# Optimization experiments

Measured on AMD Instinct MI355X. Metric: run time of the kernel, lower is better.

The kernel has to match this reference:

```python
import jax, jax.numpy as jnp
import numpy as np

B, T, D, H, L, V = 16, 1024, 512, 8, 6, 96
HS = D // H
FF = 4 * D


def setup_inputs() -> dict:
    key = jax.random.key(0)
    ks = jax.random.split(key, 16)
    n = lambda k, shape: jax.random.normal(k, shape, jnp.float32) * 0.02
    return {
        "idx": jax.random.randint(ks[0], (B, T), 0, V),
        "targets": jax.random.randint(ks[1], (B, T), 0, V),
        "tok_emb": n(ks[2], (V, D)),
        "pos_emb": n(ks[3], (T, D)),
        "Wq": n(ks[4], (L, H, D, HS)),
        "Wk": n(ks[5], (L, H, D, HS)),
        "Wv": n(ks[6], (L, H, D, HS)),
        "Wproj": n(ks[7], (L, D, D)),
        "bproj": jnp.zeros((L, D), jnp.float32),
        "W1": n(ks[8], (L, D, FF)),
        "b1": jnp.zeros((L, FF), jnp.float32),
        "W2": n(ks[9], (L, FF, D)),
        "b2": jnp.zeros((L, D), jnp.float32),
        "ln1_s": jnp.ones((L, D), jnp.float32),
        "ln1_b": jnp.zeros((L, D), jnp.float32),
        "ln2_s": jnp.ones((L, D), jnp.float32),
        "ln2_b": jnp.zeros((L, D), jnp.float32),
        "lnf_s": jnp.ones((D,), jnp.float32),
        "lnf_b": jnp.zeros((D,), jnp.float32),
        "Wout": n(ks[10], (D, V)),
        "bout": jnp.zeros((V,), jnp.float32),
    }


def _ln(x, s, b, eps=1e-5):
    m = x.mean(-1, keepdims=True)
    v = ((x - m) ** 2).mean(-1, keepdims=True)
    return (x - m) * jax.lax.rsqrt(v + eps) * s + b


def reference(idx, targets, tok_emb, pos_emb, Wq, Wk, Wv, Wproj, bproj,
              W1, b1, W2, b2, ln1_s, ln1_b, ln2_s, ln2_b, lnf_s, lnf_b,
              Wout, bout):
    x = tok_emb[idx] + pos_emb[:T]  # [B,T,D]
    causal = jnp.tril(jnp.ones((T, T), jnp.bool_))
    scale = D ** (-0.5)  # NOTE: source scales by full channel dim, not head_size
    for l in range(L):
        h = _ln(x, ln1_s[l], ln1_b[l])
        q = jnp.einsum("btd,hdk->bhtk", h, Wq[l])
        k = jnp.einsum("btd,hdk->bhtk", h, Wk[l])
        v = jnp.einsum("btd,hdk->bhtk", h, Wv[l])
        att = jnp.einsum("bhtk,bhsk->bhts", q, k) * scale
        att = jnp.where(causal, att, -jnp.inf)
        att = jax.nn.softmax(att, axis=-1)
        o = jnp.einsum("bhts,bhsk->bhtk", att, v)
        o = o.transpose(0, 2, 1, 3).reshape(B, T, D)  # concat heads
        x = x + (o @ Wproj[l] + bproj[l])
        h2 = _ln(x, ln2_s[l], ln2_b[l])
        x = x + (jnp.maximum(h2 @ W1[l] + b1[l], 0.0) @ W2[l] + b2[l])
    x = _ln(x, lnf_s, lnf_b)
    logits = (x @ Wout + bout).reshape(B * T, V)
    logp = jax.nn.log_softmax(logits, axis=-1)
    loss = -logp[jnp.arange(B * T), targets.reshape(-1)].mean()
    return logits, loss
```

## Files before the change

### kernel.cpp

```cpp
#include <hip/hip_runtime.h>

#define B_  16
#define T_  1024
#define D_  512
#define H_  8
#define L_  6
#define V_  96
#define HS_ 64
#define FF_ 2048
#define BT_ (B_*T_)
#define QKS 1024

typedef __attribute__((ext_vector_type(8))) short bf16x8;
typedef __attribute__((ext_vector_type(4))) float f32x4;

typedef __attribute__((address_space(3))) unsigned int lds_u32_t;
typedef const __attribute__((address_space(1))) unsigned int glb_u32_t;

__device__ __forceinline__ void gload16(const unsigned short* g, unsigned short* l) {
  __builtin_amdgcn_global_load_lds((glb_u32_t*)g, (lds_u32_t*)l, 16, 0, 0);
}

__device__ __forceinline__ unsigned short f2b(float f) {
  unsigned u = __float_as_uint(f);
  unsigned r = (u + 0x7FFFu + ((u >> 16) & 1u)) >> 16;
  return (unsigned short)r;
}

__global__ void zero_kernel(float* p) { p[0] = 0.f; }

__global__ __launch_bounds__(128) void embed_kernel(const int* __restrict__ idx,
    const float* __restrict__ tok, const float* __restrict__ pos, float* __restrict__ x) {
  int bt = blockIdx.x;
  int t  = bt & (T_ - 1);
  int id = idx[bt];
  if (id < 0) id = 0; if (id > V_ - 1) id = V_ - 1;
  int d  = threadIdx.x * 4;
  float4 tv = *(const float4*)(tok + (size_t)id * D_ + d);
  float4 pv = *(const float4*)(pos + (size_t)t  * D_ + d);
  float4 o = {tv.x + pv.x, tv.y + pv.y, tv.z + pv.z, tv.w + pv.w};
  *(float4*)(x + (size_t)bt * D_ + d) = o;
}

__global__ __launch_bounds__(256) void transpose_cvt(const float* __restrict__ src,
    unsigned short* __restrict__ dst, int R, int C, long sstride, long dstride,
    int zper, long zouter) {
  __shared__ float t[32][33];
  const float* s = src + (size_t)blockIdx.z * sstride;
  unsigned short* d = dst + (size_t)(blockIdx.z / zper) * zouter
                          + (size_t)(blockIdx.z % zper) * dstride;
  int r0 = blockIdx.y * 32, c0 = blockIdx.x * 32;
  int tr = threadIdx.x >> 5, tc = threadIdx.x & 31;
#pragma unroll
  for (int i = 0; i < 4; ++i)
    t[tr + i * 8][tc] = s[(size_t)(r0 + tr + i * 8) * C + c0 + tc];
  __syncthreads();
#pragma unroll
  for (int i = 0; i < 4; ++i)
    d[(size_t)(c0 + tr + i * 8) * R + r0 + tc] = f2b(t[tc][tr + i * 8]);
}

template<bool BF16OUT>
__global__ __launch_bounds__(256) void ln_kernel(const float* __restrict__ x,
    const float* __restrict__ s, const float* __restrict__ b, void* __restrict__ outv) {
  int wave = threadIdx.x >> 6;
  int lane = threadIdx.x & 63;
  int r = blockIdx.x * 4 + wave;
  const float* xr = x + (size_t)r * D_;
  float vals[8];
  float sum = 0.f;
#pragma unroll
  for (int j = 0; j < 8; ++j) { vals[j] = xr[j * 64 + lane]; sum += vals[j]; }
#pragma unroll
  for (int o = 32; o > 0; o >>= 1) sum += __shfl_xor(sum, o, 64);
  float mean = sum * (1.f / D_);
  float vs = 0.f;
#pragma unroll
  for (int j = 0; j < 8; ++j) { float d = vals[j] - mean; vs += d * d; }
#pragma unroll
  for (int o = 32; o > 0; o >>= 1) vs += __shfl_xor(vs, o, 64);
  float rstd = rsqrtf(vs * (1.f / D_) + 1e-5f);
#pragma unroll
  for (int j = 0; j < 8; ++j) {
    int c = j * 64 + lane;
    float v = (vals[j] - mean) * rstd * s[c] + b[c];
    if (BF16OUT) ((unsigned short*)outv)[(size_t)r * D_ + c] = f2b(v);
    else         ((float*)outv)[(size_t)r * D_ + c] = v;
  }
}

#define BK 32
template<bool ACC, bool RELU, bool BIAS, int OUTMODE, int MT>
__global__ __launch_bounds__(256) void mfma_gemm(
    const unsigned short* __restrict__ A,
    const unsigned short* __restrict__ Bt,
    const float* __restrict__ bias,
    void* __restrict__ Cv, void* __restrict__ Cv2,
    int K, int ldc) {
  constexpr int NI = (MT == 128) ? 4 : 2;
  constexpr int WN = (MT == 128) ? 64 : 32;
  __shared__ unsigned short Al[2][MT * BK];
  __shared__ unsigned short Bl[2][128 * BK];
  const int m0 = blockIdx.x * MT, n0 = blockIdx.y * 128;
  const int tid = threadIdx.x;
  const int lane = tid & 63, wave = tid >> 6;
  const int wy = (MT == 128) ? (wave >> 1) : 0;
  const int wx = (MT == 128) ? (wave & 1) : wave;
  const int l15 = lane & 15, quad = lane >> 4;

  const int sbase = wave * 1024;
  const int soff  = sbase + lane * 16;
  const int r0 = soff >> 6, c0e = (soff & 63) >> 1;
  const int r1 = r0 + 64;
  const int ls = sbase >> 1;
  const unsigned short* gA0 = A  + (size_t)(m0 + r0) * K + c0e;
  const unsigned short* gA1 = A  + (size_t)(m0 + r1) * K + c0e;
  const unsigned short* gB0 = Bt + (size_t)(n0 + r0) * K + c0e;
  const unsigned short* gB1 = Bt + (size_t)(n0 + r1) * K + c0e;

  auto stage = [&](int buf, int k0) {
    gload16(gA0 + k0, &Al[buf][ls]);
    if constexpr (MT == 128) gload16(gA1 + k0, &Al[buf][ls + 2048]);
    gload16(gB0 + k0, &Bl[buf][ls]);
    gload16(gB1 + k0, &Bl[buf][ls + 2048]);
  };

  f32x4 acc[4][NI];
  const f32x4 z4 = {0.f, 0.f, 0.f, 0.f};
#pragma unroll
  for (int mi = 0; mi < 4; ++mi)
#pragma unroll
    for (int ni = 0; ni < NI; ++ni) acc[mi][ni] = z4;

  stage(0, 0);
  __syncthreads();

  const int nsteps = K / BK;
  int cur = 0;
  for (int s = 0; s < nsteps; ++s) {
    if (s + 1 < nsteps) stage(cur ^ 1, (s + 1) * BK);
    bf16x8 af[4], bfr[NI];
#pragma unroll
    for (int mi = 0; mi < 4; ++mi)
      af[mi] = *(const bf16x8*)(&Al[cur][(wy * 64 + mi * 16 + l15) * BK + quad * 8]);
#pragma unroll
    for (int ni = 0; ni < NI; ++ni)
      bfr[ni] = *(const bf16x8*)(&Bl[cur][(wx * WN + ni * 16 + l15) * BK + quad * 8]);
#pragma unroll
    for (int mi = 0; mi < 4; ++mi)
#pragma unroll
      for (int ni = 0; ni < NI; ++ni)
        acc[mi][ni] = __builtin_amdgcn_mfma_f32_16x16x32_bf16(af[mi], bfr[ni], acc[mi][ni], 0, 0, 0);
    if (s + 1 < nsteps) {
      __syncthreads();
      cur ^= 1;
    }
  }

#pragma unroll
  for (int mi = 0; mi < 4; ++mi) {
    int row0 = m0 + wy * 64 + mi * 16 + quad * 4;
#pragma unroll
    for (int ni = 0; ni < NI; ++ni) {
      int col = n0 + wx * WN + ni * 16 + l15;
      float bb = BIAS ? bias[col] : 0.f;
#pragma unroll
      for (int r = 0; r < 4; ++r) {
        float v = acc[mi][ni][r] + bb;
        if (RELU) v = fmaxf(v, 0.f);
        int row = row0 + r;
        if (OUTMODE == 3) {
          if (col < 1024) {
            ((unsigned short*)Cv)[(size_t)row * QKS + col] = f2b(v);
          } else {
            int vcol = col - 1024;
            int b = row >> 10, t = row & (T_ - 1);
            int h = vcol >> 6, hs = vcol & 63;
            ((unsigned short*)Cv2)[((size_t)((b * H_ + h) * HS_ + hs)) * T_ + t] = f2b(v);
          }
        } else {
          size_t off = (size_t)row * ldc + col;
          if (ACC) v += ((const float*)Cv)[off];
          if (OUTMODE == 1) ((unsigned short*)Cv)[off] = f2b(v);
          else              ((float*)Cv)[off] = v;
        }
      }
    }
  }
}

#define PSTR 72
__global__ __launch_bounds__(256) void attn_mfma(const unsigned short* __restrict__ q,
    const unsigned short* __restrict__ k, const unsigned short* __restrict__ vt,
    unsigned short* __restrict__ o) {
  __shared__ unsigned short Pbuf[2][64 * PSTR];
  __shared__ float Lsum[4][64];
  const int bh = blockIdx.y;
  const int b = bh >> 3, hh = bh & 7;
  const int tid = threadIdx.x;
  const int lane = tid & 63, w = tid >> 6;
  const int l15 = lane & 15, quad = lane >> 4;
  const float CEXP = 0.044194173824159216f * 1.4426950408889634f;

  const unsigned short* kbase = k  + (size_t)(b * T_ + w * 16 + l15) * QKS + hh * HS_ + quad * 8;
  const unsigned short* vbase = vt + ((size_t)(bh * HS_ + w * 16 + l15)) * T_ + quad * 8;
  const int gc = w * 16 + l15;
  const f32x4 z4 = {0.f, 0.f, 0.f, 0.f};

  for (int pass = 0; pass < 2; ++pass) {
    const int qt = pass ? (int)blockIdx.x : (T_ / 64 - 1 - (int)blockIdx.x);

    bf16x8 qf[4][2];
#pragma unroll
    for (int mi = 0; mi < 4; ++mi)
#pragma unroll
      for (int c = 0; c < 2; ++c)
        qf[mi][c] = *(const bf16x8*)(q + (size_t)(b * T_ + qt * 64 + mi * 16 + l15) * QKS
                                       + hh * HS_ + c * 32 + quad * 8);

    f32x4 oacc[4];
    float psum[4][4];
#pragma unroll
    for (int mi = 0; mi < 4; ++mi) {
      oacc[mi] = z4;
#pragma unroll
      for (int r = 0; r < 4; ++r) psum[mi][r] = 0.f;
    }

    bf16x8 kf[2], vf[2];
#pragma unroll
    for (int c = 0; c < 2; ++c) {
      kf[c] = *(const bf16x8*)(kbase + c * 32);
      vf[c] = *(const bf16x8*)(vbase + c * 32);
    }

    for (int kt = 0; kt <= qt; ++kt) {
      const int ktn = (kt < qt) ? kt + 1 : qt;
      bf16x8 kfn[2], vfn[2];
#pragma unroll
      for (int c = 0; c < 2; ++c) {
        kfn[c] = *(const bf16x8*)(kbase + (size_t)ktn * 64 * QKS + c * 32);
        vfn[c] = *(const bf16x8*)(vbase + ktn * 64 + c * 32);
      }

      f32x4 s[4];
#pragma unroll
      for (int mi = 0; mi < 4; ++mi) s[mi] = z4;
      __builtin_amdgcn_s_setprio(1);
#pragma unroll
      for (int c = 0; c < 2; ++c)
#pragma unroll
        for (int mi = 0; mi < 4; ++mi)
          s[mi] = __builtin_amdgcn_mfma_f32_16x16x32_bf16(qf[mi][c], kf[c], s[mi], 0, 0, 0);
      __builtin_amdgcn_s_setprio(0);

      unsigned short* pb = Pbuf[kt & 1];
      if (kt == qt) {
#pragma unroll
        for (int mi = 0; mi < 4; ++mi)
#pragma unroll
          for (int r = 0; r < 4; ++r) {
            int row = mi * 16 + quad * 4 + r;
            float p = (gc > row) ? 0.f : exp2f(s[mi][r] * CEXP);
            unsigned short us = f2b(p);
            psum[mi][r] += __uint_as_float((unsigned)us << 16);
            pb[row * PSTR + gc] = us;
          }
      } else {
#pragma unroll
        for (int mi = 0; mi < 4; ++mi)
#pragma unroll
          for (int r = 0; r < 4; ++r) {
            int row = mi * 16 + quad * 4 + r;
            float p = exp2f(s[mi][r] * CEXP);
            unsigned short us = f2b(p);
            psum[mi][r] += __uint_as_float((unsigned)us << 16);
            pb[row * PSTR + gc] = us;
          }
      }
      __syncthreads();
      __builtin_amdgcn_s_setprio(1);
#pragma unroll
      for (int c = 0; c < 2; ++c) {
#pragma unroll
        for (int mi = 0; mi < 4; ++mi) {
          bf16x8 pf = *(const bf16x8*)(&pb[(mi * 16 + l15) * PSTR + c * 32 + quad * 8]);
          oacc[mi] = __builtin_amdgcn_mfma_f32_16x16x32_bf16(pf, vf[c], oacc[mi], 0, 0, 0);
        }
      }
      __builtin_amdgcn_s_setprio(0);
#pragma unroll
      for (int c = 0; c < 2; ++c) { kf[c] = kfn[c]; vf[c] = vfn[c]; }
    }

#pragma unroll
    for (int mi = 0; mi < 4; ++mi)
#pragma unroll
      for (int r = 0; r < 4; ++r) {
#pragma unroll
        for (int off = 1; off < 16; off <<= 1)
          psum[mi][r] += __shfl_xor(psum[mi][r], off, 64);
      }
    if (l15 == 0) {
#pragma unroll
      for (int mi = 0; mi < 4; ++mi)
#pragma unroll
        for (int r = 0; r < 4; ++r)
          Lsum[w][mi * 16 + quad * 4 + r] = psum[mi][r];
    }
    __syncthreads();
#pragma unroll
    for (int mi = 0; mi < 4; ++mi)
#pragma unroll
      for (int r = 0; r < 4; ++r) {
        int row = mi * 16 + quad * 4 + r;
        float inv = 1.f / (Lsum[0][row] + Lsum[1][row] + Lsum[2][row] + Lsum[3][row]);
        o[(size_t)(b * T_ + qt * 64 + row) * D_ + hh * HS_ + w * 16 + l15] =
            f2b(oacc[mi][r] * inv);
      }
  }
}

__global__ __launch_bounds__(256) void gemm_f32_kernel(const float* __restrict__ A, int lda,
    const float* __restrict__ Bw, int ldb, const float* __restrict__ bias,
    float* __restrict__ C, int ldc, int K, int N) {
  __shared__ float As[16][64];
  __shared__ float Bs[16][64];
  int n0 = blockIdx.y * 64;
  int nv = N - n0; if (nv > 64) nv = 64;
  int m0 = blockIdx.x * 64;
  const int tid = threadIdx.x;
  const int tx = tid & 15, ty = tid >> 4;
  const int amm = tid >> 2;
  const int akk = (tid & 3) * 4;
  const int bkk = tid >> 4;
  const int bnn = (tid & 15) * 4;
  float acc[4][4] = {};
  for (int k0 = 0; k0 < K; k0 += 16) {
    float4 av = *(const float4*)(A + (size_t)(m0 + amm) * lda + k0 + akk);
    As[akk + 0][amm] = av.x; As[akk + 1][amm] = av.y;
    As[akk + 2][amm] = av.z; As[akk + 3][amm] = av.w;
    if (bnn < nv) {
      float4 bv = *(const float4*)(Bw + (size_t)(k0 + bkk) * ldb + n0 + bnn);
      Bs[bkk][bnn + 0] = bv.x; Bs[bkk][bnn + 1] = bv.y;
      Bs[bkk][bnn + 2] = bv.z; Bs[bkk][bnn + 3] = bv.w;
    } else {
      Bs[bkk][bnn + 0] = 0.f; Bs[bkk][bnn + 1] = 0.f;
      Bs[bkk][bnn + 2] = 0.f; Bs[bkk][bnn + 3] = 0.f;
    }
    __syncthreads();
#pragma unroll
    for (int kk = 0; kk < 16; ++kk) {
      float4 a4 = *(const float4*)(&As[kk][ty * 4]);
      float4 b4 = *(const float4*)(&Bs[kk][tx * 4]);
      float aa[4] = {a4.x, a4.y, a4.z, a4.w};
      float bb[4] = {b4.x, b4.y, b4.z, b4.w};
#pragma unroll
      for (int i = 0; i < 4; ++i)
#pragma unroll
        for (int j = 0; j < 4; ++j)
          acc[i][j] = fmaf(aa[i], bb[j], acc[i][j]);
    }
    __syncthreads();
  }
  if (tx * 4 < nv) {
#pragma unroll
    for (int i = 0; i < 4; ++i) {
      float* cp = C + (size_t)(m0 + ty * 4 + i) * ldc + n0 + tx * 4;
      float4 st = {acc[i][0] + bias[n0 + tx * 4 + 0], acc[i][1] + bias[n0 + tx * 4 + 1],
                   acc[i][2] + bias[n0 + tx * 4 + 2], acc[i][3] + bias[n0 + tx * 4 + 3]};
      *(float4*)cp = st;
    }
  }
}

__global__ __launch_bounds__(256) void loss_kernel(const float* __restrict__ logits,
    const int* __restrict__ targets, float* __restrict__ loss_acc) {
  __shared__ float wsum[4];
  int wave = threadIdx.x >> 6, lane = threadIdx.x & 63;
  float local = 0.f;
  for (int r = blockIdx.x * 4 + wave; r < BT_; r += gridDim.x * 4) {
    const float* lr = logits + (size_t)r * V_;
    float v0 = lr[lane];
    float v1 = (lane < 32) ? lr[64 + lane] : -INFINITY;
    float mx = fmaxf(v0, v1);
#pragma unroll
    for (int o = 32; o > 0; o >>= 1) mx = fmaxf(mx, __shfl_xor(mx, o, 64));
    float se = expf(v0 - mx) + ((lane < 32) ? expf(v1 - mx) : 0.f);
#pragma unroll
    for (int o = 32; o > 0; o >>= 1) se += __shfl_xor(se, o, 64);
    if (lane == 0) {
      int tg = targets[r];
      if (tg < 0) tg = 0; if (tg > V_ - 1) tg = V_ - 1;
      local += (mx + logf(se)) - lr[tg];
    }
  }
  if (lane == 0) wsum[wave] = local;
  __syncthreads();
  if (threadIdx.x == 0)
    atomicAdd(loss_acc, wsum[0] + wsum[1] + wsum[2] + wsum[3]);
}

__global__ void loss_finalize_kernel(const float* __restrict__ acc, float* __restrict__ out) {
  out[(size_t)BT_ * V_] = acc[0] * (1.f / BT_);
}

static void* g_ws_fallback = nullptr;

extern "C" void kernel_launch(void* const* d_in, const int* in_sizes, int n_in,
                              void* d_out, int out_size, void* d_ws, size_t ws_size,
                              hipStream_t stream) {
  const int*   idx     = (const int*)d_in[0];
  const int*   targets = (const int*)d_in[1];
  const float* tok  = (const float*)d_in[2];
  const float* pos  = (const float*)d_in[3];
  const float* Wq   = (const float*)d_in[4];
  const float* Wk   = (const float*)d_in[5];
  const float* Wv   = (const float*)d_in[6];
  const float* Wp   = (const float*)d_in[7];
  const float* bp   = (const float*)d_in[8];
  const float* W1   = (const float*)d_in[9];
  const float* b1   = (const float*)d_in[10];
  const float* W2   = (const float*)d_in[11];
  const float* b2   = (const float*)d_in[12];
  const float* l1s  = (const float*)d_in[13];
  const float* l1b  = (const float*)d_in[14];
  const float* l2s  = (const float*)d_in[15];
  const float* l2b  = (const float*)d_in[16];
  const float* lfs  = (const float*)d_in[17];
  const float* lfb  = (const float*)d_in[18];
  const float* Wout = (const float*)d_in[19];
  const float* bout = (const float*)d_in[20];
  float* out = (float*)d_out;

  const size_t n_x  = (size_t)BT_ * D_;
  const size_t n_wT = 9437184;
  const size_t need_floats = n_x + n_x + n_x / 2 + n_x / 2 + n_x / 2 +
                             (size_t)BT_ * FF_ / 2 + n_wT + 256;
  const size_t need_bytes  = need_floats * sizeof(float);

  float* ws;
  if (ws_size >= need_bytes) {
    ws = (float*)d_ws;
  } else {
    if (!g_ws_fallback) (void)hipMalloc(&g_ws_fallback, need_bytes);
    ws = (float*)g_ws_fallback;
  }

  size_t off = 0;
  float* x  = ws + off; off += n_x;
  float* qf32 = ws + off; off += n_x;
  unsigned short* qkb = (unsigned short*)qf32;
  unsigned short* spare = (unsigned short*)(ws + off); off += n_x / 2;
  unsigned short* vtb = (unsigned short*)(ws + off); off += n_x / 2;
  unsigned short* hb  = (unsigned short*)(ws + off); off += n_x / 2;
  unsigned short* ffb = (unsigned short*)(ws + off); off += (size_t)BT_ * FF_ / 2;
  unsigned short* wqkvT = (unsigned short*)(ws + off);
  unsigned short* wpT = wqkvT + (size_t)L_ * 3 * D_ * D_;
  unsigned short* w1T = wpT + (size_t)L_ * D_ * D_;
  unsigned short* w2T = w1T + (size_t)L_ * D_ * FF_;
  off += n_wT;
  float* lacc = ws + off;
  (void)spare;

  const long DD = (long)D_ * D_;
  const long L3DD = 3 * DD;

  zero_kernel<<<1, 1, 0, stream>>>(lacc);
  embed_kernel<<<BT_, 128, 0, stream>>>(idx, tok, pos, x);

  transpose_cvt<<<dim3(2, 16, 48), 256, 0, stream>>>(Wq, wqkvT,            512, 64, 32768, 32768, 8, L3DD);
  transpose_cvt<<<dim3(2, 16, 48), 256, 0, stream>>>(Wk, wqkvT + DD,       512, 64, 32768, 32768, 8, L3DD);
  transpose_cvt<<<dim3(2, 16, 48), 256, 0, stream>>>(Wv, wqkvT + 2 * DD,   512, 64, 32768, 32768, 8, L3DD);
  transpose_cvt<<<dim3(16, 16, 6), 256, 0, stream>>>(Wp, wpT, 512, 512, 262144, 0, 1, 262144);
  transpose_cvt<<<dim3(64, 16, 6), 256, 0, stream>>>(W1, w1T, 512, 2048, 1048576, 0, 1, 1048576);
  transpose_cvt<<<dim3(16, 64, 6), 256, 0, stream>>>(W2, w2T, 2048, 512, 1048576, 0, 1, 1048576);

  const dim3 gQKV(BT_ / 128, 12);
  const dim3 gD64(BT_ / 64, D_ / 128);
  const dim3 gF(BT_ / 128, FF_ / 128);

  for (int l = 0; l < L_; ++l) {
    ln_kernel<true><<<BT_ / 4, 256, 0, stream>>>(x, l1s + (size_t)l * D_, l1b + (size_t)l * D_, hb);
    mfma_gemm<false, false, false, 3, 128><<<gQKV, 256, 0, stream>>>(
        hb, wqkvT + (size_t)l * L3DD, nullptr, qkb, vtb, D_, 0);
    attn_mfma<<<dim3(T_ / 128, B_ * H_), 256, 0, stream>>>(qkb, qkb + 512, vtb, hb);
    mfma_gemm<true, false, true, 0, 64><<<gD64, 256, 0, stream>>>(
        hb, wpT + (size_t)l * DD, bp + (size_t)l * D_, x, nullptr, D_, D_);
    ln_kernel<true><<<BT_ / 4, 256, 0, stream>>>(x, l2s + (size_t)l * D_, l2b + (size_t)l * D_, hb);
    mfma_gemm<false, true, true, 1, 128><<<gF, 256, 0, stream>>>(
        hb, w1T + (size_t)l * D_ * FF_, b1 + (size_t)l * FF_, ffb, nullptr, D_, FF_);
    mfma_gemm<true, false, true, 0, 64><<<gD64, 256, 0, stream>>>(
        ffb, w2T + (size_t)l * FF_ * D_, b2 + (size_t)l * D_, x, nullptr, FF_, D_);
  }

  ln_kernel<false><<<BT_ / 4, 256, 0, stream>>>(x, lfs, lfb, qf32);
  gemm_f32_kernel<<<dim3(BT_ / 64, 2), 256, 0, stream>>>(
      qf32, D_, Wout, V_, bout, out, V_, D_, V_);
  loss_kernel<<<64, 256, 0, stream>>>(out, targets, lacc);
  loss_finalize_kernel<<<1, 1, 0, stream>>>(lacc, out);
}
```

Before: 1.881 ms.

## Swizzle GEMM block order, pack bf16 conversion in attention, widen loss grid

The GEMM kernel remaps its flat block index with a stride-8 swizzle, with the goal of improving L2/MALL reuse across concurrently scheduled workgroups. The attention softmax merges the diagonal and off-diagonal branches and converts probabilities to bf16 in pairs using the packed hardware instruction. The row sum now accumulates the unrounded fp32 probabilities rather than the bf16-rounded values, which slightly shifts numerics. The loss kernel grid grows from 64 to 1024 blocks for more parallelism, which depends on the loss kernel handling the larger grid correctly.

```diff
diff --git a/kernel.cpp b/kernel.cpp
--- a/kernel.cpp
+++ b/kernel.cpp
@@ -101,7 +101,12 @@
   constexpr int WN = (MT == 128) ? 64 : 32;
   __shared__ unsigned short Al[2][MT * BK];
   __shared__ unsigned short Bl[2][128 * BK];
-  const int m0 = blockIdx.x * MT, n0 = blockIdx.y * 128;
+  const int nwg = gridDim.x * gridDim.y;
+  const int flat = blockIdx.x + gridDim.x * blockIdx.y;
+  const int swz = (flat & 7) * (nwg >> 3) + (flat >> 3);
+  const int bx = swz / gridDim.y;
+  const int by = swz % gridDim.y;
+  const int m0 = bx * MT, n0 = by * 128;
   const int tid = threadIdx.x;
   const int lane = tid & 63, wave = tid >> 6;
   const int wy = (MT == 128) ? (wave >> 1) : 0;
@@ -255,28 +260,26 @@
       __builtin_amdgcn_s_setprio(0);
 
       unsigned short* pb = Pbuf[kt & 1];
-      if (kt == qt) {
-#pragma unroll
-        for (int mi = 0; mi < 4; ++mi)
-#pragma unroll
-          for (int r = 0; r < 4; ++r) {
-            int row = mi * 16 + quad * 4 + r;
-            float p = (gc > row) ? 0.f : exp2f(s[mi][r] * CEXP);
-            unsigned short us = f2b(p);
-            psum[mi][r] += __uint_as_float((unsigned)us << 16);
-            pb[row * PSTR + gc] = us;
-          }
-      } else {
-#pragma unroll
-        for (int mi = 0; mi < 4; ++mi)
-#pragma unroll
-          for (int r = 0; r < 4; ++r) {
-            int row = mi * 16 + quad * 4 + r;
-            float p = exp2f(s[mi][r] * CEXP);
-            unsigned short us = f2b(p);
-            psum[mi][r] += __uint_as_float((unsigned)us << 16);
-            pb[row * PSTR + gc] = us;
-          }
+      const bool diag = (kt == qt);
+#pragma unroll
+      for (int mi = 0; mi < 4; ++mi) {
+        const int row0 = mi * 16 + quad * 4;
+        float pv_[4];
+#pragma unroll
+        for (int r = 0; r < 4; ++r) {
+          float p = exp2f(s[mi][r] * CEXP);
+          if (diag && gc > row0 + r) p = 0.f;
+          psum[mi][r] += p;
+          pv_[r] = p;
+        }
+        unsigned pk01, pk23;
+        asm("v_cvt_pk_bf16_f32 %0, %1, %2" : "=v"(pk01) : "v"(pv_[0]), "v"(pv_[1]));
+        asm("v_cvt_pk_bf16_f32 %0, %1, %2" : "=v"(pk23) : "v"(pv_[2]), "v"(pv_[3]));
+        const int base = row0 * PSTR + gc;
+        pb[base]            = (unsigned short)(pk01 & 0xFFFFu);
+        pb[base + PSTR]     = (unsigned short)(pk01 >> 16);
+        pb[base + 2 * PSTR] = (unsigned short)(pk23 & 0xFFFFu);
+        pb[base + 3 * PSTR] = (unsigned short)(pk23 >> 16);
       }
       __syncthreads();
       __builtin_amdgcn_s_setprio(1);
@@ -497,6 +500,6 @@
   ln_kernel<false><<<BT_ / 4, 256, 0, stream>>>(x, lfs, lfb, qf32);
   gemm_f32_kernel<<<dim3(BT_ / 64, 2), 256, 0, stream>>>(
       qf32, D_, Wout, V_, bout, out, V_, D_, V_);
-  loss_kernel<<<64, 256, 0, stream>>>(out, targets, lacc);
+  loss_kernel<<<1024, 256, 0, stream>>>(out, targets, lacc);
   loss_finalize_kernel<<<1, 1, 0, stream>>>(lacc, out);
 }
```

After: 1.837 ms. 1.02x faster.
